# Kernel tuning notes

Measured on AMD Instinct MI355X. Metric: run time of the kernel, lower is better.

## Reference

```python
import jax, jax.numpy as jnp
import numpy as np

J0 = 3
JBIG = 7
TH = 0.01
MM = 3.2 ** 2  # Gaussian window variance factor from get_phi


def get_phi(x):
    # phi(x) = sinc-like sin(pi x)/(pi x) * exp(-x^2/(2*mm)), with phi(0)=1
    t = jnp.pi * x
    t_safe = jnp.where(t == 0.0, 1.0, t)
    out = jnp.sin(t) * jnp.exp(-jnp.square(x) / (2.0 * MM)) / t_safe
    return jnp.where(t == 0.0, 1.0, out)


def nearest_idx(x, targets):
    # x: [N,1], targets: [K] -> index of nearest sample for each target, [K]
    return jnp.argmin(jnp.abs(x - targets[None, :]), axis=0)


def _outer_recon(wc, wr, C):
    # sum_{c,r} wc[:,c] wr[:,r] C[c,r]  (equivalent to the blockwise einsum +
    # tensordot over flattened (c,r) pairs in the torch code)
    return jnp.einsum('nc,cr,mr->nm', wc, C, wr)


def setup_inputs() -> dict:
    key = jax.random.key(0)
    k_img, k_xc, k_xr = jax.random.split(key, 3)
    N = 4096
    img = jax.random.normal(k_img, (N, N), dtype=jnp.float32)
    # sorted sample coordinates in [-1, 1] (domain spanned by wavelet translates)
    xc = jnp.sort(2.0 * jax.random.uniform(k_xc, (N, 1), dtype=jnp.float32) - 1.0, axis=0)
    xr = jnp.sort(2.0 * jax.random.uniform(k_xr, (N, 1), dtype=jnp.float32) - 1.0, axis=0)
    return {"img": img, "xc": xc, "xr": xr}


def reference(img, xc, xr):
    # ---- coarse approximation at scale j0 ----
    j0 = J0
    k = jnp.asarray(np.arange(-2 ** j0, 2 ** j0 + 1, 1), dtype=jnp.float32)  # [K0]
    phi_c = get_phi((2.0 ** j0) * xc - k[None, :])  # [N, K0]
    phi_r = get_phi((2.0 ** j0) * xr - k[None, :])  # [N, K0]
    xjk = k * (2.0 ** (-j0))
    ic = nearest_idx(xc, xjk)
    ir = nearest_idx(xr, xjk)
    F = img[ic[:, None], ir[None, :]]               # [K0, K0]
    approx = _outer_recon(phi_c, phi_r, F)          # [N, N]

    # ---- detail scales j0 .. J-1 ----
    for j in range(J0, JBIG):
        kj = jnp.asarray(np.arange((-2 ** (j + 1) - 1) / 2, 2 ** (j + 1) / 2, 0.5),
                         dtype=jnp.float32)          # [Kj] = 2^{j+2}+1
        xjk = (2.0 * kj + 1.0) * (2.0 ** (-j - 1))
        ic = nearest_idx(xc, xjk)
        ir = nearest_idx(xr, xjk)
        f = img[ic[:, None], ir[None, :]]            # [Kj, Kj]
        u = approx[ic[:, None], ir[None, :]]         # [Kj, Kj]
        diff = f - u
        # thresholded coefficient selection (torch.where -> mask, same math)
        D = jnp.where(jnp.abs(diff) > TH, diff, 0.0)
        psi_c = get_phi((2.0 ** (j + 1)) * xc - (2.0 * kj + 1.0)[None, :])  # [N, Kj]
        psi_r = get_phi((2.0 ** (j + 1)) * xr - (2.0 * kj + 1.0)[None, :])  # [N, Kj]
        approx = approx + _outer_recon(psi_c, psi_r, D)
    return approx
```

## Files before the change

kernel.cpp:

```cpp
#include <hip/hip_runtime.h>
#include <hip/hip_bf16.h>
#include <cstddef>
#include <cstdint>

#define NN 4096
#define KP 512
#define KTOT 501

typedef __attribute__((ext_vector_type(8))) short short8;
typedef __attribute__((ext_vector_type(4))) float f32x4;

#define GLB(p) ((const __attribute__((address_space(1))) void*)(p))
#define LDS(p) ((__attribute__((address_space(3))) void*)(p))

__device__ __forceinline__ float phi_eval(float x) {
    if (x == 0.0f) return 1.0f;
    const float PI_F = 3.14159265358979323846f;
    float rn = rintf(x);
    float r  = x - rn;
    float s  = __sinf(PI_F * r);
    if (((int)rn) & 1) s = -s;
    float e  = __expf(-x * x * (1.0f / 20.48f));
    return __fdividef(s * e, PI_F * x);
}

__device__ __forceinline__ void col_to_level(int col, int& l, int& off) {
    if      (col < 17)  { l = 0; off = 0;   }
    else if (col < 50)  { l = 1; off = 17;  }
    else if (col < 115) { l = 2; off = 50;  }
    else if (col < 244) { l = 3; off = 115; }
    else                { l = 4; off = 244; }
}

__device__ __forceinline__ float dot_vec(const float* __restrict__ a,
                                         const float* __restrict__ b, int n) {
    float s = 0.f;
    int k = 0;
    int head = (int)((4 - (((uintptr_t)a >> 2) & 3)) & 3);
    if (head > n) head = n;
    for (; k < head; ++k) s += a[k] * b[k];
    float s0 = 0.f, s1 = 0.f, s2 = 0.f, s3 = 0.f;
    for (; k + 4 <= n; k += 4) {
        float4 x = *(const float4*)(a + k);
        float4 y = *(const float4*)(b + k);
        s0 += x.x * y.x; s1 += x.y * y.y; s2 += x.z * y.z; s3 += x.w * y.w;
    }
    s += (s0 + s1) + (s2 + s3);
    for (; k < n; ++k) s += a[k] * b[k];
    return s;
}

__global__ void phi_kernel(const float* __restrict__ xc, const float* __restrict__ xr,
                           float* __restrict__ PhiC, float* __restrict__ PhiR) {
    int col = blockIdx.x * blockDim.x + threadIdx.x;
    int n   = blockIdx.y;
    float pc = 0.0f, pr = 0.0f;
    if (col < KTOT) {
        int l, off; col_to_level(col, l, off);
        int s = 8 << l;
        float fo = (float)(col - off - s);
        float fs = (float)s;
        pc = phi_eval(fs * xc[n] - fo);
        pr = phi_eval(fs * xr[n] - fo);
    }
    PhiC[(size_t)n * KP + col] = pc;
    PhiR[(size_t)n * KP + col] = pr;
}

__global__ void nearest_kernel(const float* __restrict__ xc, const float* __restrict__ xr,
                               int* __restrict__ idxAll) {
    int col  = blockIdx.x;
    int side = blockIdx.y;
    const float* x = side ? xr : xc;
    int l, off; col_to_level(col, l, off);
    int s = 8 << l;
    float target = (float)(col - off - s) / (float)s;

    __shared__ float sv[256];
    __shared__ int   si[256];
    int tid = threadIdx.x;
    float best = 1e30f; int bidx = 0;
    for (int n = tid; n < NN; n += 256) {
        float d = fabsf(x[n] - target);
        if (d < best) { best = d; bidx = n; }
    }
    sv[tid] = best; si[tid] = bidx;
    __syncthreads();
    for (int w = 128; w > 0; w >>= 1) {
        if (tid < w) {
            float ov = sv[tid + w]; int oi = si[tid + w];
            if (ov < sv[tid] || (ov == sv[tid] && oi < si[tid])) { sv[tid] = ov; si[tid] = oi; }
        }
        __syncthreads();
    }
    if (tid == 0) idxAll[side * KTOT + col] = si[0];
}

__global__ void zero_CdT(float* __restrict__ CdT) {
    int i = (blockIdx.x * 256 + threadIdx.x) * 4;
    *(float4*)(CdT + i) = make_float4(0.f, 0.f, 0.f, 0.f);
}

__global__ void build_C_kernel(const float* __restrict__ img, const int* __restrict__ idxAll,
                               const float* __restrict__ Usm, const float* __restrict__ PhiR,
                               float* __restrict__ CdT, int T, int off) {
    int q = blockIdx.x * 16 + threadIdx.x;
    int p = blockIdx.y * 16 + threadIdx.y;
    if (p >= T || q >= T) return;
    int ip = idxAll[off + p];
    int iq = idxAll[KTOT + off + q];
    float f = img[(size_t)ip * NN + iq];
    float val;
    if (off == 0) {
        val = f;
    } else {
        const float* Ur = Usm  + (size_t)(off + p) * KP;
        const float* Pr = PhiR + (size_t)iq * KP;
        float u = dot_vec(Ur, Pr, off);
        float d = f - u;
        val = (fabsf(d) > 0.01f) ? d : 0.0f;
    }
    CdT[(size_t)(off + q) * KP + (off + p)] = val;
}

__global__ void update_small_kernel(const float* __restrict__ PhiC, const int* __restrict__ idxAll,
                                    const float* __restrict__ CdT, float* __restrict__ Usm,
                                    int T, int off) {
    int t = blockIdx.x * 64 + threadIdx.x;
    int r = blockIdx.y * 4 + threadIdx.y;
    if (t >= T || r >= KTOT) return;
    const float* P0 = PhiC + (size_t)idxAll[r] * KP + off;
    const float* Cr = CdT  + (size_t)(off + t) * KP + off;
    Usm[(size_t)r * KP + off + t] = dot_vec(P0, Cr, T);
}

__global__ void split_kernel(const float* __restrict__ src, __hip_bfloat16* __restrict__ hi,
                             __hip_bfloat16* __restrict__ lo) {
    int i = (blockIdx.x * 256 + threadIdx.x) * 4;
    float4 v = *(const float4*)(src + i);
    __hip_bfloat16 h[4], l[4];
    float vv[4] = {v.x, v.y, v.z, v.w};
    #pragma unroll
    for (int j = 0; j < 4; ++j) {
        h[j] = __float2bfloat16(vv[j]);
        l[j] = __float2bfloat16(vv[j] - __bfloat162float(h[j]));
    }
    *(ushort4*)(hi + i) = *(const ushort4*)h;
    *(ushort4*)(lo + i) = *(const ushort4*)l;
}

#define GEMM_BODY(Ahi_, Alo_, Bhi_, Blo_)                                              \
    __shared__ short As_h[128][32];                                                    \
    __shared__ short As_l[128][32];                                                    \
    __shared__ short Bs_h[128][32];                                                    \
    __shared__ short Bs_l[128][32];                                                    \
    const int tid  = threadIdx.x;                                                      \
    const int lane = tid & 63;                                                         \
    const int wave = tid >> 6;                                                         \
    const int wr   = wave >> 1;                                                        \
    const int wc   = wave & 1;                                                         \
    const int row0 = blockIdx.y * 128;                                                 \
    const int col0 = blockIdx.x * 128;                                                 \
    f32x4 acc[4][4];                                                                   \
    _Pragma("unroll")                                                                  \
    for (int i = 0; i < 4; ++i)                                                        \
        _Pragma("unroll")                                                              \
        for (int j = 0; j < 4; ++j) acc[i][j] = (f32x4){0.f, 0.f, 0.f, 0.f};           \
    const int srow = lane >> 2;                                                        \
    const int scol = (lane & 3) * 8;                                                   \
    for (int kc = 0; kc < 16; ++kc) {                                                  \
        const int k0 = kc * 32;                                                        \
        _Pragma("unroll")                                                              \
        for (int s = 0; s < 2; ++s) {                                                  \
            const int rseg = wave * 32 + s * 16;                                       \
            const int r    = rseg + srow;                                              \
            const size_t ga = (size_t)(row0 + r) * KP + k0 + scol;                     \
            const size_t gb = (size_t)(col0 + r) * KP + k0 + scol;                     \
            __builtin_amdgcn_global_load_lds(GLB(Ahi_ + ga), LDS(&As_h[rseg][0]), 16, 0, 0); \
            __builtin_amdgcn_global_load_lds(GLB(Alo_ + ga), LDS(&As_l[rseg][0]), 16, 0, 0); \
            __builtin_amdgcn_global_load_lds(GLB(Bhi_ + gb), LDS(&Bs_h[rseg][0]), 16, 0, 0); \
            __builtin_amdgcn_global_load_lds(GLB(Blo_ + gb), LDS(&Bs_l[rseg][0]), 16, 0, 0); \
        }                                                                              \
        __syncthreads();                                                               \
        const int kb = (lane >> 4) * 8;                                                \
        short8 ah[4], al[4], bh[4], bl[4];                                             \
        _Pragma("unroll")                                                              \
        for (int mb = 0; mb < 4; ++mb) {                                               \
            const int rr = wr * 64 + mb * 16 + (lane & 15);                            \
            ah[mb] = *(const short8*)&As_h[rr][kb];                                    \
            al[mb] = *(const short8*)&As_l[rr][kb];                                    \
        }                                                                              \
        _Pragma("unroll")                                                              \
        for (int nb = 0; nb < 4; ++nb) {                                               \
            const int cc = wc * 64 + nb * 16 + (lane & 15);                            \
            bh[nb] = *(const short8*)&Bs_h[cc][kb];                                    \
            bl[nb] = *(const short8*)&Bs_l[cc][kb];                                    \
        }                                                                              \
        _Pragma("unroll")                                                              \
        for (int mb = 0; mb < 4; ++mb)                                                 \
            _Pragma("unroll")                                                          \
            for (int nb = 0; nb < 4; ++nb) {                                           \
                acc[mb][nb] = __builtin_amdgcn_mfma_f32_16x16x32_bf16(ah[mb], bh[nb], acc[mb][nb], 0, 0, 0); \
                acc[mb][nb] = __builtin_amdgcn_mfma_f32_16x16x32_bf16(ah[mb], bl[nb], acc[mb][nb], 0, 0, 0); \
                acc[mb][nb] = __builtin_amdgcn_mfma_f32_16x16x32_bf16(al[mb], bh[nb], acc[mb][nb], 0, 0, 0); \
            }                                                                          \
        __syncthreads();                                                               \
    }                                                                                  \
    const int orow = (lane >> 4) * 4;                                                  \
    const int ocol = lane & 15;

__global__ __launch_bounds__(256) void gemm_mfma_f32out(const short* __restrict__ Ahi,
                                                        const short* __restrict__ Alo,
                                                        const short* __restrict__ Bhi,
                                                        const short* __restrict__ Blo,
                                                        float* __restrict__ out) {
    GEMM_BODY(Ahi, Alo, Bhi, Blo)
    #pragma unroll
    for (int mb = 0; mb < 4; ++mb)
        #pragma unroll
        for (int nb = 0; nb < 4; ++nb) {
            const int col = col0 + wc * 64 + nb * 16 + ocol;
            #pragma unroll
            for (int reg = 0; reg < 4; ++reg) {
                const int row = row0 + wr * 64 + mb * 16 + orow + reg;
                out[(size_t)row * NN + col] = acc[mb][nb][reg];
            }
        }
}

__global__ __launch_bounds__(256) void gemm_mfma_splitout(const short* __restrict__ Ahi,
                                                          const short* __restrict__ Alo,
                                                          const short* __restrict__ Bhi,
                                                          const short* __restrict__ Blo,
                                                          unsigned short* __restrict__ Oh,
                                                          unsigned short* __restrict__ Ol) {
    GEMM_BODY(Ahi, Alo, Bhi, Blo)
    #pragma unroll
    for (int mb = 0; mb < 4; ++mb)
        #pragma unroll
        for (int nb = 0; nb < 4; ++nb) {
            const int col = col0 + wc * 64 + nb * 16 + ocol;
            #pragma unroll
            for (int reg = 0; reg < 4; ++reg) {
                const int row = row0 + wr * 64 + mb * 16 + orow + reg;
                float v = acc[mb][nb][reg];
                __hip_bfloat16 hb = __float2bfloat16(v);
                __hip_bfloat16 lb = __float2bfloat16(v - __bfloat162float(hb));
                Oh[(size_t)row * KP + col] = *(unsigned short*)&hb;
                Ol[(size_t)row * KP + col] = *(unsigned short*)&lb;
            }
        }
}

extern "C" void kernel_launch(void* const* d_in, const int* in_sizes, int n_in,
                              void* d_out, int out_size, void* d_ws, size_t ws_size,
                              hipStream_t stream) {
    const float* img = (const float*)d_in[0];
    const float* xc  = (const float*)d_in[1];
    const float* xr  = (const float*)d_in[2];
    float* out = (float*)d_out;

    const size_t M2 = (size_t)NN * KP;
    float* PhiC = (float*)d_ws;
    float* PhiR = PhiC + M2;
    float* Ubuf = PhiR + M2;
    float* CdT  = Ubuf + M2;
    float* CdTs = CdT + (size_t)KP * KP;
    int*   idxAll = (int*)(CdTs + (size_t)KP * KP);
    float* Usm  = Ubuf;
    short* PRh = (short*)Ubuf;
    short* PRl = PRh + M2;
    short* PCh = (short*)PhiR;
    short* PCl = PCh + M2;
    short* Ch  = (short*)CdTs;
    short* Cl  = Ch + (size_t)KP * KP;
    unsigned short* Uh = (unsigned short*)PhiC;
    unsigned short* Ul = Uh + M2;

    phi_kernel<<<dim3(2, NN), 256, 0, stream>>>(xc, xr, PhiC, PhiR);
    nearest_kernel<<<dim3(KTOT, 2), 256, 0, stream>>>(xc, xr, idxAll);
    zero_CdT<<<dim3(KP * KP / 1024), 256, 0, stream>>>(CdT);

    const int Ts[5]   = {17, 33, 65, 129, 257};
    const int offs[5] = {0, 17, 50, 115, 244};
    for (int l = 0; l < 5; l++) {
        dim3 bgrid((Ts[l] + 15) / 16, (Ts[l] + 15) / 16);
        build_C_kernel<<<bgrid, dim3(16, 16), 0, stream>>>(img, idxAll, Usm, PhiR, CdT,
                                                           Ts[l], offs[l]);
        if (l < 4) {
            dim3 ugrid((Ts[l] + 63) / 64, (KTOT + 3) / 4);
            update_small_kernel<<<ugrid, dim3(64, 4), 0, stream>>>(PhiC, idxAll, CdT, Usm,
                                                                   Ts[l], offs[l]);
        }
    }

    split_kernel<<<dim3((int)(M2 / 1024)), 256, 0, stream>>>(PhiR, (__hip_bfloat16*)PRh,
                                                             (__hip_bfloat16*)PRl);
    split_kernel<<<dim3((int)(M2 / 1024)), 256, 0, stream>>>(PhiC, (__hip_bfloat16*)PCh,
                                                             (__hip_bfloat16*)PCl);
    split_kernel<<<dim3(KP * KP / 1024), 256, 0, stream>>>(CdT, (__hip_bfloat16*)Ch,
                                                           (__hip_bfloat16*)Cl);

    gemm_mfma_splitout<<<dim3(KP / 128, NN / 128), 256, 0, stream>>>(PCh, PCl, Ch, Cl, Uh, Ul);

    gemm_mfma_f32out<<<dim3(NN / 128, NN / 128), 256, 0, stream>>>((const short*)Uh, (const short*)Ul,
                                                                   PRh, PRl, out);
}
```

Before: 262.6 us.

## Fuse setup, coefficient chain and bf16 splits into one cooperative persistent kernel

```diff
diff --git a/kernel.cpp b/kernel.cpp
--- a/kernel.cpp
+++ b/kernel.cpp
@@ -1,7 +1,10 @@
 #include <hip/hip_runtime.h>
 #include <hip/hip_bf16.h>
+#include <hip/hip_cooperative_groups.h>
 #include <cstddef>
 #include <cstdint>
+
+namespace cg = cooperative_groups;
 
 #define NN 4096
 #define KP 512
@@ -28,126 +31,172 @@
     if      (col < 17)  { l = 0; off = 0;   }
     else if (col < 50)  { l = 1; off = 17;  }
     else if (col < 115) { l = 2; off = 50;  }
-    else if (col < 244) { l = 3; off = 115; }
-    else                { l = 4; off = 244; }
-}
-
-__device__ __forceinline__ float dot_vec(const float* __restrict__ a,
-                                         const float* __restrict__ b, int n) {
-    float s = 0.f;
-    int k = 0;
-    int head = (int)((4 - (((uintptr_t)a >> 2) & 3)) & 3);
-    if (head > n) head = n;
-    for (; k < head; ++k) s += a[k] * b[k];
-    float s0 = 0.f, s1 = 0.f, s2 = 0.f, s3 = 0.f;
-    for (; k + 4 <= n; k += 4) {
-        float4 x = *(const float4*)(a + k);
-        float4 y = *(const float4*)(b + k);
-        s0 += x.x * y.x; s1 += x.y * y.y; s2 += x.z * y.z; s3 += x.w * y.w;
-    }
-    s += (s0 + s1) + (s2 + s3);
-    for (; k < n; ++k) s += a[k] * b[k];
-    return s;
-}
-
-__global__ void phi_kernel(const float* __restrict__ xc, const float* __restrict__ xr,
-                           float* __restrict__ PhiC, float* __restrict__ PhiR) {
-    int col = blockIdx.x * blockDim.x + threadIdx.x;
-    int n   = blockIdx.y;
-    float pc = 0.0f, pr = 0.0f;
-    if (col < KTOT) {
+    else                { l = (col < 244) ? 3 : 4; off = (col < 244) ? 115 : 244; }
+}
+
+__device__ __forceinline__ void split_bf16(float v, unsigned short& h, unsigned short& l) {
+    __hip_bfloat16 hb = __float2bfloat16(v);
+    __hip_bfloat16 lb = __float2bfloat16(v - __bfloat162float(hb));
+    h = *(unsigned short*)&hb;
+    l = *(unsigned short*)&lb;
+}
+
+
+template<int T, int OFF>
+__device__ void phase_build_C(const float* __restrict__ img, const int* __restrict__ idxAll,
+                              const float* __restrict__ Usm, const float* __restrict__ PhiR,
+                              float* __restrict__ CdT, int gid, int gthreads) {
+    for (int i = gid; i < T * T; i += gthreads) {
+        int p = i / T, q = i - p * T;
+        int ip = idxAll[OFF + p];
+        int iq = idxAll[KTOT + OFF + q];
+        float f = img[(size_t)ip * NN + iq];
+        float val;
+        if (OFF == 0) {
+            val = f;
+        } else {
+            const float* Ur = Usm  + (size_t)(OFF + p) * KP;
+            const float* Pr = PhiR + (size_t)iq * KP;
+            float s0 = 0.f, s1 = 0.f, s2 = 0.f, s3 = 0.f;
+            int k = 0;
+            #pragma unroll 4
+            for (; k + 4 <= OFF; k += 4) {
+                float4 a = *(const float4*)(Ur + k);
+                float4 b = *(const float4*)(Pr + k);
+                s0 += a.x * b.x; s1 += a.y * b.y; s2 += a.z * b.z; s3 += a.w * b.w;
+            }
+            float u = (s0 + s1) + (s2 + s3);
+            for (; k < OFF; ++k) u += Ur[k] * Pr[k];
+            float d = f - u;
+            val = (fabsf(d) > 0.01f) ? d : 0.0f;
+        }
+        CdT[(size_t)(OFF + q) * KP + (OFF + p)] = val;
+    }
+}
+
+template<int T, int OFF>
+__device__ void phase_update(const float* __restrict__ PhiC, const int* __restrict__ idxAll,
+                             const float* __restrict__ CdT, float* __restrict__ Usm,
+                             int gid, int gthreads) {
+    constexpr int HEAD = (4 - (OFF & 3)) & 3;
+    for (int i = gid; i < KTOT * T; i += gthreads) {
+        int r = i / T, t = i - r * T;
+        const float* a = PhiC + (size_t)idxAll[r] * KP + OFF;
+        const float* b = CdT  + (size_t)(OFF + t) * KP + OFF;
+        float s = 0.f;
+        int k = 0;
+        #pragma unroll
+        for (; k < HEAD; ++k) s += a[k] * b[k];
+        float s0 = 0.f, s1 = 0.f, s2 = 0.f, s3 = 0.f;
+        #pragma unroll 4
+        for (; k + 4 <= T; k += 4) {
+            float4 x = *(const float4*)(a + k);
+            float4 y = *(const float4*)(b + k);
+            s0 += x.x * y.x; s1 += x.y * y.y; s2 += x.z * y.z; s3 += x.w * y.w;
+        }
+        s += (s0 + s1) + (s2 + s3);
+        for (; k < T; ++k) s += a[k] * b[k];
+        Usm[(size_t)r * KP + OFF + t] = s;
+    }
+}
+
+__device__ void phase_split(const float* __restrict__ src, unsigned short* __restrict__ hi,
+                            unsigned short* __restrict__ lo, int ngroups, int gid, int gthreads) {
+    for (int g = gid; g < ngroups; g += gthreads) {
+        int i = g * 4;
+        float4 v = *(const float4*)(src + i);
+        unsigned short h[4], l[4];
+        split_bf16(v.x, h[0], l[0]);
+        split_bf16(v.y, h[1], l[1]);
+        split_bf16(v.z, h[2], l[2]);
+        split_bf16(v.w, h[3], l[3]);
+        *(ushort4*)(hi + i) = *(const ushort4*)h;
+        *(ushort4*)(lo + i) = *(const ushort4*)l;
+    }
+}
+
+__global__ __launch_bounds__(256, 2)
+void chain_kernel(const float* __restrict__ img, const float* __restrict__ xc,
+                  const float* __restrict__ xr,
+                  float* __restrict__ PhiC, float* __restrict__ PhiR,
+                  float* __restrict__ CdT, float* __restrict__ Usm, int* __restrict__ idxAll,
+                  unsigned short* PRh, unsigned short* PRl,
+                  unsigned short* PCh, unsigned short* PCl,
+                  unsigned short* Ch,  unsigned short* Cl) {
+    cg::grid_group grid = cg::this_grid();
+    const int tid = threadIdx.x;
+    const int bid = blockIdx.x;
+    const int gthreads = gridDim.x * 256;
+    const int gid = bid * 256 + tid;
+
+    for (int i = gid; i < NN * KP; i += gthreads) {
+        int n = i >> 9, col = i & 511;
+        float pc = 0.f, pr = 0.f;
+        if (col < KTOT) {
+            int l, off; col_to_level(col, l, off);
+            int s = 8 << l;
+            float fo = (float)(col - off - s);
+            float fs = (float)s;
+            pc = phi_eval(fs * xc[n] - fo);
+            pr = phi_eval(fs * xr[n] - fo);
+        }
+        PhiC[i] = pc;
+        PhiR[i] = pr;
+    }
+    for (int i = gid; i < KP * KP; i += gthreads) CdT[i] = 0.f;
+    __shared__ float sv[256];
+    __shared__ int   si[256];
+    for (int task = bid; task < 2 * KTOT; task += gridDim.x) {
+        int side = (task >= KTOT);
+        int col  = side ? task - KTOT : task;
+        const float* x = side ? xr : xc;
         int l, off; col_to_level(col, l, off);
         int s = 8 << l;
-        float fo = (float)(col - off - s);
-        float fs = (float)s;
-        pc = phi_eval(fs * xc[n] - fo);
-        pr = phi_eval(fs * xr[n] - fo);
-    }
-    PhiC[(size_t)n * KP + col] = pc;
-    PhiR[(size_t)n * KP + col] = pr;
-}
-
-__global__ void nearest_kernel(const float* __restrict__ xc, const float* __restrict__ xr,
-                               int* __restrict__ idxAll) {
-    int col  = blockIdx.x;
-    int side = blockIdx.y;
-    const float* x = side ? xr : xc;
-    int l, off; col_to_level(col, l, off);
-    int s = 8 << l;
-    float target = (float)(col - off - s) / (float)s;
-
-    __shared__ float sv[256];
-    __shared__ int   si[256];
-    int tid = threadIdx.x;
-    float best = 1e30f; int bidx = 0;
-    for (int n = tid; n < NN; n += 256) {
-        float d = fabsf(x[n] - target);
-        if (d < best) { best = d; bidx = n; }
-    }
-    sv[tid] = best; si[tid] = bidx;
-    __syncthreads();
-    for (int w = 128; w > 0; w >>= 1) {
-        if (tid < w) {
-            float ov = sv[tid + w]; int oi = si[tid + w];
-            if (ov < sv[tid] || (ov == sv[tid] && oi < si[tid])) { sv[tid] = ov; si[tid] = oi; }
-        }
+        float target = (float)(col - off - s) / (float)s;
+        float best = 1e30f; int bidx = 0;
+        for (int n = tid; n < NN; n += 256) {
+            float d = fabsf(x[n] - target);
+            if (d < best) { best = d; bidx = n; }
+        }
+        sv[tid] = best; si[tid] = bidx;
         __syncthreads();
-    }
-    if (tid == 0) idxAll[side * KTOT + col] = si[0];
-}
-
-__global__ void zero_CdT(float* __restrict__ CdT) {
-    int i = (blockIdx.x * 256 + threadIdx.x) * 4;
-    *(float4*)(CdT + i) = make_float4(0.f, 0.f, 0.f, 0.f);
-}
-
-__global__ void build_C_kernel(const float* __restrict__ img, const int* __restrict__ idxAll,
-                               const float* __restrict__ Usm, const float* __restrict__ PhiR,
-                               float* __restrict__ CdT, int T, int off) {
-    int q = blockIdx.x * 16 + threadIdx.x;
-    int p = blockIdx.y * 16 + threadIdx.y;
-    if (p >= T || q >= T) return;
-    int ip = idxAll[off + p];
-    int iq = idxAll[KTOT + off + q];
-    float f = img[(size_t)ip * NN + iq];
-    float val;
-    if (off == 0) {
-        val = f;
-    } else {
-        const float* Ur = Usm  + (size_t)(off + p) * KP;
-        const float* Pr = PhiR + (size_t)iq * KP;
-        float u = dot_vec(Ur, Pr, off);
-        float d = f - u;
-        val = (fabsf(d) > 0.01f) ? d : 0.0f;
-    }
-    CdT[(size_t)(off + q) * KP + (off + p)] = val;
-}
-
-__global__ void update_small_kernel(const float* __restrict__ PhiC, const int* __restrict__ idxAll,
-                                    const float* __restrict__ CdT, float* __restrict__ Usm,
-                                    int T, int off) {
-    int t = blockIdx.x * 64 + threadIdx.x;
-    int r = blockIdx.y * 4 + threadIdx.y;
-    if (t >= T || r >= KTOT) return;
-    const float* P0 = PhiC + (size_t)idxAll[r] * KP + off;
-    const float* Cr = CdT  + (size_t)(off + t) * KP + off;
-    Usm[(size_t)r * KP + off + t] = dot_vec(P0, Cr, T);
-}
-
-__global__ void split_kernel(const float* __restrict__ src, __hip_bfloat16* __restrict__ hi,
-                             __hip_bfloat16* __restrict__ lo) {
-    int i = (blockIdx.x * 256 + threadIdx.x) * 4;
-    float4 v = *(const float4*)(src + i);
-    __hip_bfloat16 h[4], l[4];
-    float vv[4] = {v.x, v.y, v.z, v.w};
-    #pragma unroll
-    for (int j = 0; j < 4; ++j) {
-        h[j] = __float2bfloat16(vv[j]);
-        l[j] = __float2bfloat16(vv[j] - __bfloat162float(h[j]));
-    }
-    *(ushort4*)(hi + i) = *(const ushort4*)h;
-    *(ushort4*)(lo + i) = *(const ushort4*)l;
-}
+        for (int w = 128; w > 0; w >>= 1) {
+            if (tid < w) {
+                float ov = sv[tid + w]; int oi = si[tid + w];
+                if (ov < sv[tid] || (ov == sv[tid] && oi < si[tid])) { sv[tid] = ov; si[tid] = oi; }
+            }
+            __syncthreads();
+        }
+        if (tid == 0) idxAll[task] = si[0];
+        __syncthreads();
+    }
+    grid.sync();
+
+    phase_build_C<17, 0>(img, idxAll, Usm, PhiR, CdT, gid, gthreads);
+    grid.sync();
+    phase_update<17, 0>(PhiC, idxAll, CdT, Usm, gid, gthreads);
+    grid.sync();
+    phase_build_C<33, 17>(img, idxAll, Usm, PhiR, CdT, gid, gthreads);
+    grid.sync();
+    phase_update<33, 17>(PhiC, idxAll, CdT, Usm, gid, gthreads);
+    grid.sync();
+    phase_build_C<65, 50>(img, idxAll, Usm, PhiR, CdT, gid, gthreads);
+    grid.sync();
+    phase_update<65, 50>(PhiC, idxAll, CdT, Usm, gid, gthreads);
+    grid.sync();
+    phase_build_C<129, 115>(img, idxAll, Usm, PhiR, CdT, gid, gthreads);
+    grid.sync();
+    phase_update<129, 115>(PhiC, idxAll, CdT, Usm, gid, gthreads);
+    grid.sync();
+    phase_build_C<257, 244>(img, idxAll, Usm, PhiR, CdT, gid, gthreads);
+    grid.sync();
+
+    phase_split(PhiR, PRh, PRl, NN * KP / 4, gid, gthreads);
+    phase_split(CdT,  Ch,  Cl,  KP * KP / 4, gid, gthreads);
+    grid.sync();
+    phase_split(PhiC, PCh, PCl, NN * KP / 4, gid, gthreads);
+}
+
 
 #define GEMM_BODY(Ahi_, Alo_, Bhi_, Blo_)                                              \
     __shared__ short As_h[128][32];                                                    \
@@ -243,11 +292,10 @@
             #pragma unroll
             for (int reg = 0; reg < 4; ++reg) {
                 const int row = row0 + wr * 64 + mb * 16 + orow + reg;
-                float v = acc[mb][nb][reg];
-                __hip_bfloat16 hb = __float2bfloat16(v);
-                __hip_bfloat16 lb = __float2bfloat16(v - __bfloat162float(hb));
-                Oh[(size_t)row * KP + col] = *(unsigned short*)&hb;
-                Ol[(size_t)row * KP + col] = *(unsigned short*)&lb;
+                unsigned short h, l;
+                split_bf16(acc[mb][nb][reg], h, l);
+                Oh[(size_t)row * KP + col] = h;
+                Ol[(size_t)row * KP + col] = l;
             }
         }
 }
@@ -268,41 +316,25 @@
     float* CdTs = CdT + (size_t)KP * KP;
     int*   idxAll = (int*)(CdTs + (size_t)KP * KP);
     float* Usm  = Ubuf;
-    short* PRh = (short*)Ubuf;
-    short* PRl = PRh + M2;
-    short* PCh = (short*)PhiR;
-    short* PCl = PCh + M2;
-    short* Ch  = (short*)CdTs;
-    short* Cl  = Ch + (size_t)KP * KP;
-    unsigned short* Uh = (unsigned short*)PhiC;
-    unsigned short* Ul = Uh + M2;
-
-    phi_kernel<<<dim3(2, NN), 256, 0, stream>>>(xc, xr, PhiC, PhiR);
-    nearest_kernel<<<dim3(KTOT, 2), 256, 0, stream>>>(xc, xr, idxAll);
-    zero_CdT<<<dim3(KP * KP / 1024), 256, 0, stream>>>(CdT);
-
-    const int Ts[5]   = {17, 33, 65, 129, 257};
-    const int offs[5] = {0, 17, 50, 115, 244};
-    for (int l = 0; l < 5; l++) {
-        dim3 bgrid((Ts[l] + 15) / 16, (Ts[l] + 15) / 16);
-        build_C_kernel<<<bgrid, dim3(16, 16), 0, stream>>>(img, idxAll, Usm, PhiR, CdT,
-                                                           Ts[l], offs[l]);
-        if (l < 4) {
-            dim3 ugrid((Ts[l] + 63) / 64, (KTOT + 3) / 4);
-            update_small_kernel<<<ugrid, dim3(64, 4), 0, stream>>>(PhiC, idxAll, CdT, Usm,
-                                                                   Ts[l], offs[l]);
-        }
-    }
-
-    split_kernel<<<dim3((int)(M2 / 1024)), 256, 0, stream>>>(PhiR, (__hip_bfloat16*)PRh,
-                                                             (__hip_bfloat16*)PRl);
-    split_kernel<<<dim3((int)(M2 / 1024)), 256, 0, stream>>>(PhiC, (__hip_bfloat16*)PCh,
-                                                             (__hip_bfloat16*)PCl);
-    split_kernel<<<dim3(KP * KP / 1024), 256, 0, stream>>>(CdT, (__hip_bfloat16*)Ch,
-                                                           (__hip_bfloat16*)Cl);
-
-    gemm_mfma_splitout<<<dim3(KP / 128, NN / 128), 256, 0, stream>>>(PCh, PCl, Ch, Cl, Uh, Ul);
-
-    gemm_mfma_f32out<<<dim3(NN / 128, NN / 128), 256, 0, stream>>>((const short*)Uh, (const short*)Ul,
-                                                                   PRh, PRl, out);
-}
+    unsigned short* PRh = (unsigned short*)Ubuf;
+    unsigned short* PRl = PRh + M2;
+    unsigned short* PCh = (unsigned short*)PhiR;
+    unsigned short* PCl = PCh + M2;
+    unsigned short* Ch  = (unsigned short*)CdTs;
+    unsigned short* Cl  = Ch + (size_t)KP * KP;
+    unsigned short* Uh  = (unsigned short*)PhiC;
+    unsigned short* Ul  = Uh + M2;
+
+    void* args[] = { (void*)&img, (void*)&xc, (void*)&xr,
+                     (void*)&PhiC, (void*)&PhiR, (void*)&CdT, (void*)&Usm, (void*)&idxAll,
+                     (void*)&PRh, (void*)&PRl, (void*)&PCh, (void*)&PCl,
+                     (void*)&Ch, (void*)&Cl };
+    hipLaunchCooperativeKernel(reinterpret_cast<void*>(chain_kernel),
+                               dim3(512), dim3(256), args, 0, stream);
+
+    gemm_mfma_splitout<<<dim3(KP / 128, NN / 128), 256, 0, stream>>>(
+        (const short*)PCh, (const short*)PCl, (const short*)Ch, (const short*)Cl, Uh, Ul);
+
+    gemm_mfma_f32out<<<dim3(NN / 128, NN / 128), 256, 0, stream>>>(
+        (const short*)Uh, (const short*)Ul, (const short*)PRh, (const short*)PRl, out);
+}
```

Result: slower. 831.9 us (+216.7%).
